# Optimization experiments

Measured on AMD Instinct MI355X. Metric: run time of the kernel, lower is better.

The kernel has to match this reference:

```python
import jax, jax.numpy as jnp
import numpy as np

N, T, D, H = 100000, 16, 8, 40
HP1 = H + 1
ALPHA_DP = 1.0
KAPPA0 = 1000.0   # priorGaussianVarKappa
NU0 = 100.0       # priorWishartNu
PSI0_SCALE = 500.0  # priorWishartPsi = 500*I


def setup_inputs() -> dict:
    key = jax.random.key(0)
    ks = jax.random.split(key, 6)
    return {
        "BetaGamma1": jnp.ones((1, T), jnp.float32),
        "Phi": jax.random.uniform(ks[0], (N, T), jnp.float32),
        "inputData": jax.random.normal(ks[1], (N, D), jnp.float32),
        "outputData": jax.random.normal(ks[2], (N, 1), jnp.float32),
        "weightELM": jax.random.uniform(ks[3], (D, H), jnp.float32) * 2.0 - 1.0,
        "biasELM": jax.random.normal(ks[4], (H, 1), jnp.float32),
        "epsilonA": jnp.ones((1, T), jnp.float32),
        "epsilonB": jnp.ones((1, T), jnp.float32),
        "zetaA": 1e-4 * jnp.ones((1, T), jnp.float32),
        "zetaB": jnp.ones((1, T), jnp.float32),
    }


def reference(BetaGamma1, Phi, inputData, outputData, weightELM, biasELM,
              epsilonA, epsilonB, zetaA, zetaB):
    f32 = jnp.float32
    mu0 = jnp.zeros((D, 1), f32)                      # priorGaussianMeanMu
    Psi0 = PSI0_SCALE * jnp.eye(D, dtype=f32)         # priorWishartPsi

    sumPhi = jnp.sum(Phi, axis=0, keepdims=True)      # [1,T]

    # stick-breaking Beta params. Torch builds a flipped [T,N,T] tril mask;
    # mathematically BetaGamma2[t] = alpha + sum_{j>t} sum_n Phi[n,j]
    BetaGamma1_new = jnp.ones_like(BetaGamma1) + sumPhi
    col = sumPhi[0]                                   # [T]
    rev_incl = jnp.cumsum(col[::-1])[::-1]            # sum_{j>=t}
    BetaGamma2 = (ALPHA_DP + (rev_incl - col))[None, :]

    # Gaussian-Wishart natural-parameter updates.
    # Torch loops over clusters doing [N,D,D] bmm outer products; this is
    # S[:,:,t] = sum_n Phi[n,t] x_n x_n^T
    S = jnp.einsum('nt,ni,nj->ijt', Phi, inputData, inputData)  # [D,D,T]
    t11 = -0.5 * (Psi0 + KAPPA0 * mu0 @ mu0.T)[:, :, None] - 0.5 * S
    t12 = KAPPA0 * mu0 + inputData.T @ Phi            # [D,T]
    t21 = -0.5 * sumPhi - 0.5 * (NU0 + D + 2)         # [1,T]
    kappa = KAPPA0 + sumPhi                           # [1,T]
    mu = t12 / kappa                                  # [D,T]
    nu = -2.0 * t21 - 2.0 - float(D)                  # [1,T]
    psi = -2.0 * t11 - kappa[0][None, None, :] * jnp.einsum('it,jt->ijt', mu, mu)

    # ELM feature map + augmented design matrix X = [sigmoid(x W + b), 1]
    hmap = jax.nn.sigmoid(inputData @ weightELM + biasELM.T)   # [N,H]
    X = jnp.concatenate([hmap, jnp.ones((inputData.shape[0], 1), f32)], axis=1)  # [N,HP1]

    epsExp = (epsilonA / epsilonB)[0]                 # [T]
    zetaExp = (zetaA / zetaB)[0]                      # [T]

    # A[t] = X^T diag(Phi[:,t]) X   (torch: per-cluster bmm with diag_embed)
    A = jnp.einsum('nt,ni,nj->tij', Phi, X, X)        # [T,HP1,HP1]
    WS = jnp.linalg.inv(epsExp[:, None, None] * A
                        + zetaExp[:, None, None] * jnp.eye(HP1, dtype=f32))
    # b[t] = X^T diag(Phi[:,t]) y
    b = jnp.einsum('ni,nt->ti', X * outputData, Phi)  # [T,HP1]
    WMv = zetaExp[:, None] * jnp.einsum('tij,tj->ti', WS, b)   # [T,HP1]
    WM = WMv[:, :, None]                              # [T,HP1,1]

    # prior Zeta/Epsilon alias the variational initial values in __init__
    zetaA_new = zetaA + (H + 1) * 0.5
    zetaB_new = zetaB + 0.5 * (jnp.sum(WMv * WMv, axis=1)
                               + jnp.trace(WS, axis1=-2, axis2=-1))[None, :]
    epsA_new = epsilonA + 0.5 * sumPhi

    pred = jnp.einsum('ni,ti->tn', X, WMv)            # [T,N]
    err = outputData.T - pred                          # [T,N]
    t1 = jnp.einsum('tn,nt->t', err * err, Phi)[None, :]
    t2 = jnp.einsum('tij,tji->t', A, WS)[None, :]
    epsB_new = epsilonB + 0.5 * (t1 + t2)

    return (BetaGamma1_new, BetaGamma2, mu, kappa, nu, psi,
            WM, WS, zetaA_new, zetaB_new, epsA_new, epsB_new)
```

## Files before the change

### kernel.cpp

```cpp
#include <hip/hip_runtime.h>

#define Nn 100000
#define Tt 16
#define Dd 8
#define Hh 40
#define HP1 41
#define XSD 51
#define PSD 16
#define NPAIR 1275
#define NB 128
#define NTILES ((Nn + NB - 1) / NB)
#define SLAB 20480
#define MAXSLABS 784
#define SLABGRP 64
#define MAXGRP ((MAXSLABS + SLABGRP - 1) / SLABGRP)
#define WS_ACC 0
#define WS_PART 21504
#define WS_SLB (WS_PART + MAXGRP * SLAB)

#define OFF_BG1   0
#define OFF_BG2   16
#define OFF_MU    32
#define OFF_KAPPA 160
#define OFF_NU    176
#define OFF_PSI   192
#define OFF_WM    1216
#define OFF_WS    1872
#define OFF_ZA    28768
#define OFF_ZB    28784
#define OFF_EA    28800
#define OFF_EB    28816

typedef float v16f __attribute__((ext_vector_type(16)));

__device__ __forceinline__ int pidx(int i, int j) {
  if (i > j) { int tmp = i; i = j; j = tmp; }
  return (i * (2 * 50 - i + 1)) / 2 + (j - i);
}

__device__ __forceinline__ void fma16(v16f& A, float p, float4 q0, float4 q1,
                                      float4 q2, float4 q3) {
  A[0]  = fmaf(p, q0.x, A[0]);  A[1]  = fmaf(p, q0.y, A[1]);
  A[2]  = fmaf(p, q0.z, A[2]);  A[3]  = fmaf(p, q0.w, A[3]);
  A[4]  = fmaf(p, q1.x, A[4]);  A[5]  = fmaf(p, q1.y, A[5]);
  A[6]  = fmaf(p, q1.z, A[6]);  A[7]  = fmaf(p, q1.w, A[7]);
  A[8]  = fmaf(p, q2.x, A[8]);  A[9]  = fmaf(p, q2.y, A[9]);
  A[10] = fmaf(p, q2.z, A[10]); A[11] = fmaf(p, q2.w, A[11]);
  A[12] = fmaf(p, q3.x, A[12]); A[13] = fmaf(p, q3.y, A[13]);
  A[14] = fmaf(p, q3.z, A[14]); A[15] = fmaf(p, q3.w, A[15]);
}

__global__ __launch_bounds__(256, 3)
void gram_reduce(const float* __restrict__ Phi, const float* __restrict__ Xd,
                 const float* __restrict__ Yd, const float* __restrict__ Welm,
                 const float* __restrict__ belm, float* __restrict__ slabs)
{
  __shared__ float sW[Dd * Hh];
  __shared__ float sb[Hh];
  __shared__ float Xs[NB][XSD];
  __shared__ __align__(16) float Ps[NB][PSD];

  int tid = threadIdx.x;
  for (int i = tid; i < Dd * Hh; i += 256) sW[i] = Welm[i];
  if (tid < Hh) sb[tid] = belm[tid];

  int rp = -1, cq = 0;
  {
    int c = 0;
    for (int r = 0; r < 25; ++r) {
      int cmin = (2 * r) / 3;
      int cnt = 17 - cmin;
      if (rp < 0 && tid < c + cnt) { rp = r; cq = cmin + (tid - c); }
      c += cnt;
    }
    if (tid >= c) rp = -1;
  }
  bool active = (rp >= 0);
  int r0 = 2 * rp, r1 = 2 * rp + 1;
  int c0 = 3 * cq, c1 = 3 * cq + 1, c2 = 3 * cq + 2;
  if (!active) { r0 = r1 = 0; c0 = c1 = c2 = 0; }

  v16f A00 = {}, A01 = {}, A02 = {}, A10 = {}, A11 = {}, A12 = {};

  for (int tile = blockIdx.x; tile < NTILES; tile += gridDim.x) {
    int n0 = tile * NB;
    __syncthreads();
    for (int idx = tid; idx < NB * 4; idx += 256) {
      int n = idx >> 2, q = idx & 3;
      int gn = n0 + n;
      ((float4*)&Ps[n][0])[q] = (gn < Nn)
        ? ((const float4*)(Phi + (size_t)gn * Tt))[q]
        : make_float4(0.f, 0.f, 0.f, 0.f);
    }
    for (int idx = tid; idx < NB * Dd; idx += 256) {
      int n = idx / Dd, d = idx % Dd;
      int gn = n0 + n;
      Xs[n][41 + d] = (gn < Nn) ? Xd[gn * Dd + d] : 0.f;
    }
    for (int n = tid; n < NB; n += 256) {
      int gn = n0 + n;
      Xs[n][49] = (gn < Nn) ? Yd[gn] : 0.f;
      Xs[n][40] = (gn < Nn) ? 1.f : 0.f;
      Xs[n][50] = 0.f;
    }
    __syncthreads();
    for (int idx = tid; idx < NB * Hh; idx += 256) {
      int n = idx / Hh, h = idx % Hh;
      float z = sb[h];
#pragma unroll
      for (int d = 0; d < Dd; ++d) z += Xs[n][41 + d] * sW[d * Hh + h];
      float s = 1.f / (1.f + __expf(-z));
      Xs[n][h] = (n0 + n < Nn) ? s : 0.f;
    }
    __syncthreads();
    if (active) {
#pragma unroll 2
      for (int n = 0; n < NB; ++n) {
        const float4* pr = (const float4*)&Ps[n][0];
        float4 q0 = pr[0], q1 = pr[1], q2 = pr[2], q3 = pr[3];
        float xi0 = Xs[n][r0], xi1 = Xs[n][r1];
        float xj0 = Xs[n][c0], xj1 = Xs[n][c1], xj2 = Xs[n][c2];
        fma16(A00, xi0 * xj0, q0, q1, q2, q3);
        fma16(A01, xi0 * xj1, q0, q1, q2, q3);
        fma16(A02, xi0 * xj2, q0, q1, q2, q3);
        fma16(A10, xi1 * xj0, q0, q1, q2, q3);
        fma16(A11, xi1 * xj1, q0, q1, q2, q3);
        fma16(A12, xi1 * xj2, q0, q1, q2, q3);
      }
    }
  }
  float* slab = slabs + (size_t)blockIdx.x * SLAB;
  if (active) {
    if (c0 >= r0 && c0 < 50) *(v16f*)(slab + pidx(r0, c0) * Tt) = A00;
    if (c1 >= r0 && c1 < 50) *(v16f*)(slab + pidx(r0, c1) * Tt) = A01;
    if (c2 >= r0 && c2 < 50) *(v16f*)(slab + pidx(r0, c2) * Tt) = A02;
    if (c0 >= r1 && c0 < 50) *(v16f*)(slab + pidx(r1, c0) * Tt) = A10;
    if (c1 >= r1 && c1 < 50) *(v16f*)(slab + pidx(r1, c1) * Tt) = A11;
    if (c2 >= r1 && c2 < 50) *(v16f*)(slab + pidx(r1, c2) * Tt) = A12;
  }
}

__global__ __launch_bounds__(256)
void reduce_slabs_a(const float4* __restrict__ slabs4, int nslabs,
                    float4* __restrict__ part4)
{
  int g = blockIdx.y;
  int idx = blockIdx.x * 256 + threadIdx.x;
  int b0 = g * SLABGRP;
  int b1 = b0 + SLABGRP; if (b1 > nslabs) b1 = nslabs;
  float4 s = make_float4(0.f, 0.f, 0.f, 0.f);
  for (int b = b0; b < b1; ++b) {
    float4 v = slabs4[(size_t)b * (SLAB / 4) + idx];
    s.x += v.x; s.y += v.y; s.z += v.z; s.w += v.w;
  }
  part4[(size_t)g * (SLAB / 4) + idx] = s;
}

__global__ __launch_bounds__(256)
void reduce_slabs_b(const float4* __restrict__ part4, int ngrp,
                    float4* __restrict__ accout4)
{
  int idx = blockIdx.x * 256 + threadIdx.x;
  float4 s = make_float4(0.f, 0.f, 0.f, 0.f);
  for (int g = 0; g < ngrp; ++g) {
    float4 v = part4[(size_t)g * (SLAB / 4) + idx];
    s.x += v.x; s.y += v.y; s.z += v.z; s.w += v.w;
  }
  accout4[idx] = s;
}

__global__ __launch_bounds__(256)
void finalize_kernel(const float* __restrict__ acc, const float* __restrict__ epsA,
                     const float* __restrict__ epsB, const float* __restrict__ zetA,
                     const float* __restrict__ zetB, float* __restrict__ out)
{
  int t = blockIdx.x;
  int tid = threadIdx.x;
  __shared__ float G[HP1][84];
  __shared__ float As[HP1][HP1 + 1];
  __shared__ float bs[HP1];
  __shared__ float colk[HP1];
  __shared__ float red[256];
  __shared__ float wmv[HP1];
  __shared__ float rowv[4][HP1 + 1];
  __shared__ float mus[Dd];

  float epsExp = epsA[t] / epsB[t];
  float zetaExp = zetA[t] / zetB[t];

  for (int idx = tid; idx < HP1 * HP1; idx += 256) {
    int i = idx / HP1, j = idx % HP1;
    float a = acc[pidx(i, j) * Tt + t];
    As[i][j] = a;
    G[i][j] = epsExp * a + (i == j ? zetaExp : 0.f);
    G[i][41 + j] = (i == j) ? 1.f : 0.f;
  }
  for (int idx = tid; idx < HP1; idx += 256) {
    G[idx][82] = 0.f; G[idx][83] = 0.f;
    bs[idx] = acc[pidx(idx, 49) * Tt + t];
  }
  __syncthreads();

  int c = tid % HP1;
  int ig = tid / HP1;
  int irow0 = ig * 7;

  for (int k = 0; k < HP1; ++k) {
    float pivinv = 1.f / G[k][k];
    if (tid >= 1 && tid <= HP1) G[k][k + tid] *= pivinv;
    if (tid < HP1) colk[tid] = (tid == k) ? 0.f : G[tid][k];
    __syncthreads();
    if (ig < 6) {
      int j = k + 1 + c;
      float pk = G[k][j];
#pragma unroll
      for (int r = 0; r < 7; ++r) {
        int i = irow0 + r;
        if (i < HP1 && i != k) G[i][j] = fmaf(-colk[i], pk, G[i][j]);
      }
    }
    __syncthreads();
  }

  for (int idx = tid; idx < HP1 * HP1; idx += 256) {
    int i = idx / HP1, j = idx % HP1;
    out[OFF_WS + (t * HP1 + i) * HP1 + j] = G[i][41 + j];
  }
  if (tid < HP1) {
    float s = 0.f;
    for (int j = 0; j < HP1; ++j) s += G[tid][41 + j] * bs[j];
    float w = zetaExp * s;
    wmv[tid] = w;
    out[OFF_WM + t * HP1 + tid] = w;
  }
  __syncthreads();
  float lt2 = 0.f;
  for (int idx = tid; idx < HP1 * HP1; idx += 256) {
    int i = idx / HP1, j = idx % HP1;
    lt2 += As[i][j] * G[i][41 + j];
  }
  red[tid] = lt2; __syncthreads();
  for (int s = 128; s > 0; s >>= 1) {
    if (tid < s) red[tid] += red[tid + s];
    __syncthreads();
  }
  float t2v = red[0];
  if (tid < HP1) {
    float w = wmv[tid];
    float aw = 0.f;
    for (int j = 0; j < HP1; ++j) aw += As[tid][j] * wmv[j];
    rowv[0][tid] = w * bs[tid];
    rowv[1][tid] = w * w;
    rowv[2][tid] = G[tid][41 + tid];
    rowv[3][tid] = w * aw;
  }
  __syncthreads();

  float sp = acc[pidx(40, 40) * Tt + t];
  float kap = 1000.f + sp;
  float syy = acc[pidx(49, 49) * Tt + t];

  if (tid == 0) {
    float wb = 0.f, wn = 0.f, trc = 0.f, quad = 0.f;
    for (int i = 0; i < HP1; ++i) {
      wb += rowv[0][i]; wn += rowv[1][i]; trc += rowv[2][i]; quad += rowv[3][i];
    }
    float t1 = syy - 2.f * wb + quad;
    out[OFF_BG1 + t] = 1.f + sp;
    float rest = 0.f;
    for (int u = t + 1; u < Tt; ++u) rest += acc[pidx(40, 40) * Tt + u];
    out[OFF_BG2 + t] = 1.f + rest;
    out[OFF_KAPPA + t] = kap;
    out[OFF_NU + t] = sp + 100.f;
    out[OFF_ZA + t] = zetA[t] + 0.5f * (float)HP1;
    out[OFF_ZB + t] = zetB[t] + 0.5f * (wn + trc);
    out[OFF_EA + t] = epsA[t] + 0.5f * sp;
    out[OFF_EB + t] = epsB[t] + 0.5f * (t1 + t2v);
  }
  if (tid < Dd) {
    float m = acc[pidx(40, 41 + tid) * Tt + t] / kap;
    mus[tid] = m;
    out[OFF_MU + tid * Tt + t] = m;
  }
  __syncthreads();
  if (tid < Dd * Dd) {
    int i = tid / Dd, j = tid % Dd;
    float S = acc[pidx(41 + i, 41 + j) * Tt + t];
    float v = (i == j ? 500.f : 0.f) + S - kap * mus[i] * mus[j];
    out[OFF_PSI + (i * Dd + j) * Tt + t] = v;
  }
}

extern "C" void kernel_launch(void* const* d_in, const int* in_sizes, int n_in,
                              void* d_out, int out_size, void* d_ws, size_t ws_size,
                              hipStream_t stream) {
  const float* Phi = (const float*)d_in[1];
  const float* Xd  = (const float*)d_in[2];
  const float* Yd  = (const float*)d_in[3];
  const float* W   = (const float*)d_in[4];
  const float* bb  = (const float*)d_in[5];
  const float* eA  = (const float*)d_in[6];
  const float* eB  = (const float*)d_in[7];
  const float* zA  = (const float*)d_in[8];
  const float* zB  = (const float*)d_in[9];
  float* out = (float*)d_out;
  float* ws  = (float*)d_ws;

  float* acc_red = ws + WS_ACC;
  float* part    = ws + WS_PART;
  float* slabs   = ws + WS_SLB;

  long avail = (long)(ws_size / 4) - WS_SLB;
  int grid1 = (int)(avail / SLAB);
  if (grid1 > NTILES) grid1 = NTILES;
  if (grid1 > MAXSLABS) grid1 = MAXSLABS;
  if (grid1 < 1) grid1 = 1;
  int ngrp = (grid1 + SLABGRP - 1) / SLABGRP;

  hipLaunchKernelGGL(gram_reduce, dim3(grid1), dim3(256), 0, stream, Phi, Xd, Yd, W, bb, slabs);
  hipLaunchKernelGGL(reduce_slabs_a, dim3(SLAB / 4 / 256, ngrp), dim3(256), 0, stream,
                     (const float4*)slabs, grid1, (float4*)part);
  hipLaunchKernelGGL(reduce_slabs_b, dim3(SLAB / 4 / 256), dim3(256), 0, stream,
                     (const float4*)part, ngrp, (float4*)acc_red);
  hipLaunchKernelGGL(finalize_kernel, dim3(Tt), dim3(256), 0, stream, acc_red, eA, eB, zA, zB, out);
}
```

Before: 206.8 us.

## Compute weighted Gram matrices with split-fp16 MFMA over a precomputed ELM expansion

Replaces the scalar-FMA Gram accumulation with a two-stage scheme. A first kernel expands each sample into a 64-wide row (sigmoid features, bias, inputs, output), stored as packed fp16 hi/lo pairs. A second kernel forms the Phi-weighted products with 16x16x32 fp16 MFMA, using three hi/lo cross terms to approximate fp32 accuracy. Chunk partials are written in an [i][t][j] layout, reduced once, and the final 16-way sum is folded into the finalize kernel. This trades a large extra global write and read (about 25 MB) and some precision risk for matrix-core throughput.

```diff
diff --git a/kernel.cpp b/kernel.cpp
--- a/kernel.cpp
+++ b/kernel.cpp
@@ -5,18 +5,14 @@
 #define Dd 8
 #define Hh 40
 #define HP1 41
-#define XSD 51
-#define PSD 16
-#define NPAIR 1275
-#define NB 128
-#define NTILES ((Nn + NB - 1) / NB)
-#define SLAB 20480
-#define MAXSLABS 784
-#define SLABGRP 64
-#define MAXGRP ((MAXSLABS + SLABGRP - 1) / SLABGRP)
-#define WS_ACC 0
-#define WS_PART 21504
-#define WS_SLB (WS_PART + MAXGRP * SLAB)
+
+#define CSZ 53248
+#define KCMAX 125
+#define XE_PAIR_OFF 0
+#define XE_PAIR_SZ  (Nn * 64)
+#define PART_OFF    (XE_PAIR_OFF + XE_PAIR_SZ)
+#define PART_SZ     (16 * CSZ)
+#define P_OFF       (PART_OFF + PART_SZ)
 
 #define OFF_BG1   0
 #define OFF_BG2   16
@@ -31,146 +27,182 @@
 #define OFF_EA    28800
 #define OFF_EB    28816
 
-typedef float v16f __attribute__((ext_vector_type(16)));
-
-__device__ __forceinline__ int pidx(int i, int j) {
-  if (i > j) { int tmp = i; i = j; j = tmp; }
-  return (i * (2 * 50 - i + 1)) / 2 + (j - i);
-}
-
-__device__ __forceinline__ void fma16(v16f& A, float p, float4 q0, float4 q1,
-                                      float4 q2, float4 q3) {
-  A[0]  = fmaf(p, q0.x, A[0]);  A[1]  = fmaf(p, q0.y, A[1]);
-  A[2]  = fmaf(p, q0.z, A[2]);  A[3]  = fmaf(p, q0.w, A[3]);
-  A[4]  = fmaf(p, q1.x, A[4]);  A[5]  = fmaf(p, q1.y, A[5]);
-  A[6]  = fmaf(p, q1.z, A[6]);  A[7]  = fmaf(p, q1.w, A[7]);
-  A[8]  = fmaf(p, q2.x, A[8]);  A[9]  = fmaf(p, q2.y, A[9]);
-  A[10] = fmaf(p, q2.z, A[10]); A[11] = fmaf(p, q2.w, A[11]);
-  A[12] = fmaf(p, q3.x, A[12]); A[13] = fmaf(p, q3.y, A[13]);
-  A[14] = fmaf(p, q3.z, A[14]); A[15] = fmaf(p, q3.w, A[15]);
-}
-
-__global__ __launch_bounds__(256, 3)
-void gram_reduce(const float* __restrict__ Phi, const float* __restrict__ Xd,
-                 const float* __restrict__ Yd, const float* __restrict__ Welm,
-                 const float* __restrict__ belm, float* __restrict__ slabs)
+typedef _Float16 f16x8 __attribute__((ext_vector_type(8)));
+typedef float f32x4 __attribute__((ext_vector_type(4)));
+typedef unsigned short u16x8 __attribute__((ext_vector_type(8)));
+
+#define AIDX(i, t, j) ((((i) * 16 + (t)) * 64) + (j))
+
+__global__ __launch_bounds__(256)
+void elm_expand(const float* __restrict__ Xd, const float* __restrict__ Yd,
+                const float* __restrict__ W, const float* __restrict__ bb,
+                unsigned int* __restrict__ XePair)
 {
   __shared__ float sW[Dd * Hh];
   __shared__ float sb[Hh];
-  __shared__ float Xs[NB][XSD];
-  __shared__ __align__(16) float Ps[NB][PSD];
-
+  __shared__ float xs[64][9];
+  __shared__ float ys[64];
+  __shared__ float hrow[64][41];
   int tid = threadIdx.x;
-  for (int i = tid; i < Dd * Hh; i += 256) sW[i] = Welm[i];
-  if (tid < Hh) sb[tid] = belm[tid];
-
-  int rp = -1, cq = 0;
+  int n0 = blockIdx.x * 64;
+
+  for (int i = tid; i < Dd * Hh; i += 256) sW[i] = W[i];
+  if (tid < Hh) sb[tid] = bb[tid];
+  if (tid < 128) {
+    int nl = tid >> 1, h4 = (tid & 1) * 4;
+    int gn = n0 + nl;
+    float4 v = (gn < Nn) ? *(const float4*)(Xd + (size_t)gn * 8 + h4)
+                         : make_float4(0.f, 0.f, 0.f, 0.f);
+    xs[nl][h4 + 0] = v.x; xs[nl][h4 + 1] = v.y;
+    xs[nl][h4 + 2] = v.z; xs[nl][h4 + 3] = v.w;
+  }
+  if (tid < 64) { int gn = n0 + tid; ys[tid] = (gn < Nn) ? Yd[gn] : 0.f; }
+  __syncthreads();
+
   {
-    int c = 0;
-    for (int r = 0; r < 25; ++r) {
-      int cmin = (2 * r) / 3;
-      int cnt = 17 - cmin;
-      if (rp < 0 && tid < c + cnt) { rp = r; cq = cmin + (tid - c); }
-      c += cnt;
-    }
-    if (tid >= c) rp = -1;
-  }
-  bool active = (rp >= 0);
-  int r0 = 2 * rp, r1 = 2 * rp + 1;
-  int c0 = 3 * cq, c1 = 3 * cq + 1, c2 = 3 * cq + 2;
-  if (!active) { r0 = r1 = 0; c0 = c1 = c2 = 0; }
-
-  v16f A00 = {}, A01 = {}, A02 = {}, A10 = {}, A11 = {}, A12 = {};
-
-  for (int tile = blockIdx.x; tile < NTILES; tile += gridDim.x) {
-    int n0 = tile * NB;
-    __syncthreads();
-    for (int idx = tid; idx < NB * 4; idx += 256) {
-      int n = idx >> 2, q = idx & 3;
-      int gn = n0 + n;
-      ((float4*)&Ps[n][0])[q] = (gn < Nn)
-        ? ((const float4*)(Phi + (size_t)gn * Tt))[q]
-        : make_float4(0.f, 0.f, 0.f, 0.f);
-    }
-    for (int idx = tid; idx < NB * Dd; idx += 256) {
-      int n = idx / Dd, d = idx % Dd;
-      int gn = n0 + n;
-      Xs[n][41 + d] = (gn < Nn) ? Xd[gn * Dd + d] : 0.f;
-    }
-    for (int n = tid; n < NB; n += 256) {
-      int gn = n0 + n;
-      Xs[n][49] = (gn < Nn) ? Yd[gn] : 0.f;
-      Xs[n][40] = (gn < Nn) ? 1.f : 0.f;
-      Xs[n][50] = 0.f;
-    }
-    __syncthreads();
-    for (int idx = tid; idx < NB * Hh; idx += 256) {
-      int n = idx / Hh, h = idx % Hh;
+    int nl = tid >> 2, hq = (tid & 3) * 10;
+    for (int hh = 0; hh < 10; ++hh) {
+      int h = hq + hh;
       float z = sb[h];
 #pragma unroll
-      for (int d = 0; d < Dd; ++d) z += Xs[n][41 + d] * sW[d * Hh + h];
-      float s = 1.f / (1.f + __expf(-z));
-      Xs[n][h] = (n0 + n < Nn) ? s : 0.f;
-    }
-    __syncthreads();
-    if (active) {
-#pragma unroll 2
-      for (int n = 0; n < NB; ++n) {
-        const float4* pr = (const float4*)&Ps[n][0];
-        float4 q0 = pr[0], q1 = pr[1], q2 = pr[2], q3 = pr[3];
-        float xi0 = Xs[n][r0], xi1 = Xs[n][r1];
-        float xj0 = Xs[n][c0], xj1 = Xs[n][c1], xj2 = Xs[n][c2];
-        fma16(A00, xi0 * xj0, q0, q1, q2, q3);
-        fma16(A01, xi0 * xj1, q0, q1, q2, q3);
-        fma16(A02, xi0 * xj2, q0, q1, q2, q3);
-        fma16(A10, xi1 * xj0, q0, q1, q2, q3);
-        fma16(A11, xi1 * xj1, q0, q1, q2, q3);
-        fma16(A12, xi1 * xj2, q0, q1, q2, q3);
-      }
-    }
-  }
-  float* slab = slabs + (size_t)blockIdx.x * SLAB;
-  if (active) {
-    if (c0 >= r0 && c0 < 50) *(v16f*)(slab + pidx(r0, c0) * Tt) = A00;
-    if (c1 >= r0 && c1 < 50) *(v16f*)(slab + pidx(r0, c1) * Tt) = A01;
-    if (c2 >= r0 && c2 < 50) *(v16f*)(slab + pidx(r0, c2) * Tt) = A02;
-    if (c0 >= r1 && c0 < 50) *(v16f*)(slab + pidx(r1, c0) * Tt) = A10;
-    if (c1 >= r1 && c1 < 50) *(v16f*)(slab + pidx(r1, c1) * Tt) = A11;
-    if (c2 >= r1 && c2 < 50) *(v16f*)(slab + pidx(r1, c2) * Tt) = A12;
+      for (int d = 0; d < 8; ++d) z = fmaf(xs[nl][d], sW[d * Hh + h], z);
+      hrow[nl][h] = 1.f / (1.f + __expf(-z));
+    }
+  }
+  __syncthreads();
+
+  for (int pass = 0; pass < 16; ++pass) {
+    int idx = pass * 256 + tid;
+    int nl = idx >> 6, cc = idx & 63;
+    int gn = n0 + nl;
+    if (gn < Nn) {
+      float v = (cc < Hh) ? hrow[nl][cc]
+              : (cc == 40) ? 1.f
+              : (cc < 49) ? xs[nl][cc - 41]
+              : (cc == 49) ? ys[nl] : 0.f;
+      _Float16 hi = (_Float16)v;
+      _Float16 lo = (_Float16)(v - (float)hi);
+      unsigned int u = ((unsigned int)__builtin_bit_cast(unsigned short, lo) << 16)
+                     |  (unsigned int)__builtin_bit_cast(unsigned short, hi);
+      XePair[(size_t)gn * 64 + cc] = u;
+    }
+  }
+}
+
+__device__ __forceinline__ float pair_to_f32(unsigned int u) {
+  _Float16 hi = __builtin_bit_cast(_Float16, (unsigned short)(u & 0xffffu));
+  _Float16 lo = __builtin_bit_cast(_Float16, (unsigned short)(u >> 16));
+  return (float)hi + (float)lo;
+}
+
+__global__ __launch_bounds__(256, 2)
+void gram_mfma(const float* __restrict__ Phi, const unsigned int* __restrict__ XePair,
+               float* __restrict__ P, int CH)
+{
+  int tid = threadIdx.x;
+  int lane = tid & 63;
+  int wave = tid >> 6;
+  int wg_n = wave & 1;
+  int wg_m = wave >> 1;
+  int l15 = lane & 15, lg = lane >> 4;
+  int bM = blockIdx.x;
+  int c  = blockIdx.y;
+  int n0 = c * CH;
+  int nEnd = n0 + CH; if (nEnd > Nn) nEnd = Nn;
+  int i0 = bM * 13 + wg_m * 7;
+  int jB = wg_n * 32 + l15;
+
+  f32x4 acc[7][2];
+#pragma unroll
+  for (int m = 0; m < 7; ++m) {
+    acc[m][0] = (f32x4){0.f, 0.f, 0.f, 0.f};
+    acc[m][1] = (f32x4){0.f, 0.f, 0.f, 0.f};
+  }
+
+  for (int nb = n0; nb < nEnd; nb += 32) {
+    int kb = nb + lg * 8;
+
+    float ph[8];
+#pragma unroll
+    for (int e = 0; e < 8; ++e) ph[e] = Phi[(size_t)(kb + e) * 16 + l15];
+
+    f16x8 bh[2], bl[2];
+#pragma unroll
+    for (int nt = 0; nt < 2; ++nt) {
+      u16x8 vh, vl;
+#pragma unroll
+      for (int e = 0; e < 8; ++e) {
+        unsigned int u = XePair[(size_t)(kb + e) * 64 + jB + nt * 16];
+        vh[e] = (unsigned short)(u & 0xffffu);
+        vl[e] = (unsigned short)(u >> 16);
+      }
+      bh[nt] = __builtin_bit_cast(f16x8, vh);
+      bl[nt] = __builtin_bit_cast(f16x8, vl);
+    }
+
+#pragma unroll
+    for (int mt = 0; mt < 7; ++mt) {
+      int iA = i0 + mt;
+      f16x8 ah, al;
+#pragma unroll
+      for (int e = 0; e < 8; ++e) {
+        unsigned int u = XePair[(size_t)(kb + e) * 64 + iA];
+        float a = ph[e] * pair_to_f32(u);
+        _Float16 h = (_Float16)a;
+        ah[e] = h;
+        al[e] = (_Float16)(a - (float)h);
+      }
+#pragma unroll
+      for (int nt = 0; nt < 2; ++nt) {
+        acc[mt][nt] = __builtin_amdgcn_mfma_f32_16x16x32_f16(ah, bh[nt], acc[mt][nt], 0, 0, 0);
+        acc[mt][nt] = __builtin_amdgcn_mfma_f32_16x16x32_f16(ah, bl[nt], acc[mt][nt], 0, 0, 0);
+        acc[mt][nt] = __builtin_amdgcn_mfma_f32_16x16x32_f16(al, bh[nt], acc[mt][nt], 0, 0, 0);
+      }
+    }
+  }
+
+  int ntile = (wg_m == 1) ? 6 : 7;
+  float* Pc = P + (size_t)c * CSZ;
+#pragma unroll
+  for (int mt = 0; mt < 7; ++mt) {
+    if (mt >= ntile) break;
+    int iA = i0 + mt;
+#pragma unroll
+    for (int nt = 0; nt < 2; ++nt) {
+      int j = wg_n * 32 + nt * 16 + l15;
+#pragma unroll
+      for (int r = 0; r < 4; ++r) {
+        Pc[(iA * 16 + (lg * 4 + r)) * 64 + j] = acc[mt][nt][r];
+      }
+    }
   }
 }
 
 __global__ __launch_bounds__(256)
-void reduce_slabs_a(const float4* __restrict__ slabs4, int nslabs,
-                    float4* __restrict__ part4)
+void reduce_chunks(const float4* __restrict__ P4, int nchunks, float4* __restrict__ part4)
 {
   int g = blockIdx.y;
   int idx = blockIdx.x * 256 + threadIdx.x;
-  int b0 = g * SLABGRP;
-  int b1 = b0 + SLABGRP; if (b1 > nslabs) b1 = nslabs;
+  int per = (nchunks + 15) / 16;
+  int c0 = g * per;
+  int c1 = c0 + per; if (c1 > nchunks) c1 = nchunks;
   float4 s = make_float4(0.f, 0.f, 0.f, 0.f);
-  for (int b = b0; b < b1; ++b) {
-    float4 v = slabs4[(size_t)b * (SLAB / 4) + idx];
+  for (int cc = c0; cc < c1; ++cc) {
+    float4 v = P4[(size_t)cc * (CSZ / 4) + idx];
     s.x += v.x; s.y += v.y; s.z += v.z; s.w += v.w;
   }
-  part4[(size_t)g * (SLAB / 4) + idx] = s;
+  part4[(size_t)g * (CSZ / 4) + idx] = s;
+}
+
+__device__ __forceinline__ float accv(const float* __restrict__ part, int idx) {
+  float s = 0.f;
+#pragma unroll
+  for (int g = 0; g < 16; ++g) s += part[g * CSZ + idx];
+  return s;
 }
 
 __global__ __launch_bounds__(256)
-void reduce_slabs_b(const float4* __restrict__ part4, int ngrp,
-                    float4* __restrict__ accout4)
-{
-  int idx = blockIdx.x * 256 + threadIdx.x;
-  float4 s = make_float4(0.f, 0.f, 0.f, 0.f);
-  for (int g = 0; g < ngrp; ++g) {
-    float4 v = part4[(size_t)g * (SLAB / 4) + idx];
-    s.x += v.x; s.y += v.y; s.z += v.z; s.w += v.w;
-  }
-  accout4[idx] = s;
-}
-
-__global__ __launch_bounds__(256)
-void finalize_kernel(const float* __restrict__ acc, const float* __restrict__ epsA,
+void finalize_kernel(const float* __restrict__ part, const float* __restrict__ epsA,
                      const float* __restrict__ epsB, const float* __restrict__ zetA,
                      const float* __restrict__ zetB, float* __restrict__ out)
 {
@@ -190,14 +222,14 @@
 
   for (int idx = tid; idx < HP1 * HP1; idx += 256) {
     int i = idx / HP1, j = idx % HP1;
-    float a = acc[pidx(i, j) * Tt + t];
+    float a = accv(part, AIDX(i, t, j));
     As[i][j] = a;
     G[i][j] = epsExp * a + (i == j ? zetaExp : 0.f);
     G[i][41 + j] = (i == j) ? 1.f : 0.f;
   }
   for (int idx = tid; idx < HP1; idx += 256) {
     G[idx][82] = 0.f; G[idx][83] = 0.f;
-    bs[idx] = acc[pidx(idx, 49) * Tt + t];
+    bs[idx] = accv(part, AIDX(idx, t, 49));
   }
   __syncthreads();
 
@@ -256,9 +288,9 @@
   }
   __syncthreads();
 
-  float sp = acc[pidx(40, 40) * Tt + t];
+  float sp = accv(part, AIDX(40, t, 40));
   float kap = 1000.f + sp;
-  float syy = acc[pidx(49, 49) * Tt + t];
+  float syy = accv(part, AIDX(49, t, 49));
 
   if (tid == 0) {
     float wb = 0.f, wn = 0.f, trc = 0.f, quad = 0.f;
@@ -268,7 +300,7 @@
     float t1 = syy - 2.f * wb + quad;
     out[OFF_BG1 + t] = 1.f + sp;
     float rest = 0.f;
-    for (int u = t + 1; u < Tt; ++u) rest += acc[pidx(40, 40) * Tt + u];
+    for (int u = t + 1; u < Tt; ++u) rest += accv(part, AIDX(40, u, 40));
     out[OFF_BG2 + t] = 1.f + rest;
     out[OFF_KAPPA + t] = kap;
     out[OFF_NU + t] = sp + 100.f;
@@ -278,14 +310,14 @@
     out[OFF_EB + t] = epsB[t] + 0.5f * (t1 + t2v);
   }
   if (tid < Dd) {
-    float m = acc[pidx(40, 41 + tid) * Tt + t] / kap;
+    float m = accv(part, AIDX(40, t, 41 + tid)) / kap;
     mus[tid] = m;
     out[OFF_MU + tid * Tt + t] = m;
   }
   __syncthreads();
   if (tid < Dd * Dd) {
     int i = tid / Dd, j = tid % Dd;
-    float S = acc[pidx(41 + i, 41 + j) * Tt + t];
+    float S = accv(part, AIDX(41 + i, t, 41 + j));
     float v = (i == j ? 500.f : 0.f) + S - kap * mus[i] * mus[j];
     out[OFF_PSI + (i * Dd + j) * Tt + t] = v;
   }
@@ -306,21 +338,22 @@
   float* out = (float*)d_out;
   float* ws  = (float*)d_ws;
 
-  float* acc_red = ws + WS_ACC;
-  float* part    = ws + WS_PART;
-  float* slabs   = ws + WS_SLB;
-
-  long avail = (long)(ws_size / 4) - WS_SLB;
-  int grid1 = (int)(avail / SLAB);
-  if (grid1 > NTILES) grid1 = NTILES;
-  if (grid1 > MAXSLABS) grid1 = MAXSLABS;
-  if (grid1 < 1) grid1 = 1;
-  int ngrp = (grid1 + SLABGRP - 1) / SLABGRP;
-
-  hipLaunchKernelGGL(gram_reduce, dim3(grid1), dim3(256), 0, stream, Phi, Xd, Yd, W, bb, slabs);
-  hipLaunchKernelGGL(reduce_slabs_a, dim3(SLAB / 4 / 256, ngrp), dim3(256), 0, stream,
-                     (const float4*)slabs, grid1, (float4*)part);
-  hipLaunchKernelGGL(reduce_slabs_b, dim3(SLAB / 4 / 256), dim3(256), 0, stream,
-                     (const float4*)part, ngrp, (float4*)acc_red);
-  hipLaunchKernelGGL(finalize_kernel, dim3(Tt), dim3(256), 0, stream, acc_red, eA, eB, zA, zB, out);
-}
+  unsigned int* XePair = (unsigned int*)(ws + XE_PAIR_OFF);
+  float* part = ws + PART_OFF;
+  float* P    = ws + P_OFF;
+
+  long maxChunks = ((long)(ws_size / 4) - (long)P_OFF) / CSZ;
+  int mch = 1;
+  while (mch < KCMAX && (long)((KCMAX + mch - 1) / mch) > maxChunks) ++mch;
+  int CH = 800 * mch;
+  int KCe = (Nn + CH - 1) / CH;
+
+  hipLaunchKernelGGL(elm_expand, dim3((Nn + 63) / 64), dim3(256), 0, stream,
+                     Xd, Yd, W, bb, XePair);
+  hipLaunchKernelGGL(gram_mfma, dim3(4, KCe), dim3(256), 0, stream,
+                     Phi, XePair, P, CH);
+  hipLaunchKernelGGL(reduce_chunks, dim3(52, 16), dim3(256), 0, stream,
+                     (const float4*)P, KCe, (float4*)part);
+  hipLaunchKernelGGL(finalize_kernel, dim3(Tt), dim3(256), 0, stream,
+                     part, eA, eB, zA, zB, out);
+}
```

Measured after the change: 202.3 us. 1.02x faster.
